# Kernel optimization log

Measured on AMD Instinct MI355X. Metric: run time of the kernel, lower is better.

## Reference

```python
import jax, jax.numpy as jnp
import numpy as np

HEADS = 8
DIM_HEAD = 64
EPS = 1e-5  # fp32 eps in ChanLayerNorm


def chan_layer_norm(x, g):
    # x: [b, c, h, w]; normalize over channel dim with biased variance
    mean = jnp.mean(x, axis=1, keepdims=True)
    var = jnp.var(x, axis=1, keepdims=True)
    return (x - mean) * jax.lax.rsqrt(var + EPS) * g[None, :, None, None]


def setup_inputs() -> dict:
    key = jax.random.key(0)
    k1, k2, k3 = jax.random.split(key, 3)
    dim, inner = 512, HEADS * DIM_HEAD
    fmap = jax.random.normal(k1, (16, dim, 64, 64), dtype=jnp.float32)
    # 1x1 conv weights (no bias); scaled like typical init to keep softmax unsaturated
    w_qkv = jax.random.normal(k2, (3 * inner, dim), dtype=jnp.float32) * 0.02
    w_out = jax.random.normal(k3, (dim, inner), dtype=jnp.float32) * 0.02
    g1 = jnp.ones((dim,), dtype=jnp.float32)
    g2 = jnp.ones((dim,), dtype=jnp.float32)
    return {"fmap": fmap, "g1": g1, "w_qkv": w_qkv, "w_out": w_out, "g2": g2}


def reference(fmap, g1, w_qkv, w_out, g2):
    b, c, X, Y = fmap.shape
    h, dh = HEADS, DIM_HEAD
    n = X * Y  # seq_len
    scale = dh ** -0.5

    x = chan_layer_norm(fmap, g1)
    # 1x1 conv == channel matmul: [b, 3*inner, X, Y]
    qkv = jnp.einsum('bcxy,oc->boxy', x, w_qkv)
    q, k, v = jnp.split(qkv, 3, axis=1)

    def to_bhnc(t):
        # b (h c) x y -> b h n c
        return t.reshape(b, h, dh, n).transpose(0, 1, 3, 2)

    q, k, v = map(to_bhnc, (q, k, v))

    q = jax.nn.softmax(q, axis=-1) * scale          # softmax over feature dim
    k = jax.nn.softmax(k, axis=2)                   # softmax over seq dim
    v = v / jnp.linalg.norm(v, axis=-1, keepdims=True)  # l2norm
    inv_sqrt_n = 1.0 / np.sqrt(n)
    k = k * inv_sqrt_n
    v = v * inv_sqrt_n

    context = jnp.einsum('bhnd,bhne->bhde', k, v)   # small d x e context
    out = jnp.einsum('bhnd,bhde->bhne', q, context)  # [b, h, n, dh]

    # b h n d -> b (h d) x y
    out = out.transpose(0, 1, 3, 2).reshape(b, h * dh, X, Y)
    out = jax.nn.gelu(out, approximate=False)
    out = jnp.einsum('bcxy,oc->boxy', out, w_out)
    return chan_layer_norm(out, g2)
```

## Files before the change

### kernel.cpp

```cpp
#include <hip/hip_runtime.h>

typedef unsigned short u16;
typedef __attribute__((ext_vector_type(2))) float f32x2;
typedef __attribute__((ext_vector_type(4))) float f32x4;
typedef __attribute__((ext_vector_type(8))) short s16x8;
typedef __attribute__((ext_vector_type(8))) u16 u16x8;
typedef __attribute__((ext_vector_type(4))) u16 u16x4;

#define NB 16
#define CD 512
#define NS 4096
#define NHD 8

#define SBAR  __builtin_amdgcn_s_barrier()
#define SCHED __builtin_amdgcn_sched_barrier(0)
#define LGKM0 asm volatile("s_waitcnt lgkmcnt(0)" ::: "memory")
#define PRIO1 __builtin_amdgcn_s_setprio(1)
#define PRIO0 __builtin_amdgcn_s_setprio(0)

__device__ __forceinline__ float bf2f(u16 u){
  union { unsigned int i; float f; } z; z.i = ((unsigned int)u) << 16; return z.f;
}
__device__ __forceinline__ u16 f2bf(float f){
  union { float f; unsigned int i; } z; z.f = f;
  unsigned int i = z.i;
  return (u16)((i + 0x7fffu + ((i >> 16) & 1u)) >> 16);
}
__device__ __forceinline__ float gelu_f(float x){
  return 0.5f * x * (1.0f + erff(x * 0.70710678118654752440f));
}
__device__ __forceinline__ void gl_lds16(const u16* g, u16* l){
  __builtin_amdgcn_global_load_lds((const __attribute__((address_space(1))) void*)(g),
                                   (__attribute__((address_space(3))) void*)(l), 16, 0, 0);
}

__global__ void prep_w_k(const float* __restrict__ wqkv, const float* __restrict__ g1,
                         const float* __restrict__ wout, u16* __restrict__ w1b,
                         u16* __restrict__ w2b){
  int i = blockIdx.x * 256 + threadIdx.x;
  if (i < 1536*512) {
    w1b[i] = f2bf(wqkv[i] * g1[i & 511]);
  } else {
    int j = i - 1536*512;
    w2b[j] = f2bf(wout[j]);
  }
}

__global__ __launch_bounds__(512) void ln1t_k(const float* __restrict__ fmap,
                                              u16* __restrict__ xlnT){
  int b = blockIdx.y, n0 = blockIdx.x * 32;
  int t = threadIdx.x;
  int lane = t & 63, wv = t >> 6;
  __shared__ float Lb[512][36];
  __shared__ u16 Tt[64][36];
  __shared__ float red1[8][8][4], red2[8][8][4];
  __shared__ float mean_s[32], rstd_s[32];

  int ng = t & 7;
  float s1[4] = {0,0,0,0}, s2[4] = {0,0,0,0};
  const float* fb = fmap + ((size_t)b*CD)*NS + n0 + ng*4;
  #pragma unroll
  for (int it = 0; it < 8; ++it){
    int q = it*512 + t;
    int c = q >> 3;
    f32x4 v = *(const f32x4*)&fb[(size_t)c*NS];
    *(f32x4*)&Lb[c][ng*4] = v;
    #pragma unroll
    for (int j = 0; j < 4; ++j){ s1[j] += v[j]; s2[j] += v[j]*v[j]; }
  }
  #pragma unroll
  for (int off = 8; off < 64; off <<= 1)
    #pragma unroll
    for (int j = 0; j < 4; ++j){
      s1[j] += __shfl_xor(s1[j], off, 64);
      s2[j] += __shfl_xor(s2[j], off, 64);
    }
  if (lane < 8){
    #pragma unroll
    for (int j = 0; j < 4; ++j){ red1[wv][lane][j] = s1[j]; red2[wv][lane][j] = s2[j]; }
  }
  __syncthreads();
  if (t < 32){
    int g = t >> 2, j = t & 3;
    float a = 0.f, bq = 0.f;
    #pragma unroll
    for (int w = 0; w < 8; ++w){ a += red1[w][g][j]; bq += red2[w][g][j]; }
    float mn = a * (1.f/512.f);
    float var = bq * (1.f/512.f) - mn*mn;
    mean_s[t] = mn; rstd_s[t] = rsqrtf(var + 1e-5f);
  }
  __syncthreads();

  for (int ct = 0; ct < 8; ++ct){
    {
      int cl = t >> 3, n4 = (t & 7) * 4;
      f32x4 v = *(const f32x4*)&Lb[ct*64 + cl][n4];
      u16x4 pk;
      #pragma unroll
      for (int j = 0; j < 4; ++j)
        pk[j] = f2bf((v[j] - mean_s[n4+j]) * rstd_s[n4+j]);
      *(u16x4*)&Tt[cl][n4] = pk;
    }
    __syncthreads();
    {
      int nr = t >> 4, c4 = t & 15;
      u16x4 w;
      #pragma unroll
      for (int j = 0; j < 4; ++j) w[j] = Tt[c4*4 + j][nr];
      *(u16x4*)&xlnT[((size_t)b*NS + n0 + nr)*CD + ct*64 + c4*4] = w;
    }
    __syncthreads();
  }
}

__global__ __launch_bounds__(512, 2) void gemm1_k(const u16* __restrict__ A,
                                                  const u16* __restrict__ Bm,
                                                  u16* __restrict__ Cm){
  __shared__ u16 lds[4][16384];
  int bi = blockIdx.x;
  int xcd = bi & 7, r2 = bi >> 3;
  int gi = r2 / 6, yy = r2 - gi*6;
  int g  = gi*8 + xcd;
  int x  = g & 15, z = g >> 4;
  int o0 = yy*256, bn0 = x*256;
  int t = threadIdx.x;
  int lane = t & 63, wv = t >> 6;
  int wm = wv >> 2, wn = wv & 3;
  int fr = lane & 15, fg = lane >> 4;
  const u16* Ab = A + (size_t)o0*512;
  const u16* Bb = Bm + ((size_t)z*NS + bn0)*512;
  int rA = t >> 2, cx = t & 3;

  f32x4 acc[8][4];
  #pragma unroll
  for (int i=0;i<8;++i)
    #pragma unroll
    for (int j=0;j<4;++j) acc[i][j] = (f32x4){0.f,0.f,0.f,0.f};
  s16x8 afr[4], bfr[4];

  auto stA = [&](int slot, int kt, int bt){
    int r = bt*128 + rA;
    gl_lds16(Ab + (size_t)r*512 + kt + ((cx ^ (r&3))<<3), &lds[slot][bt*4096 + wv*512]);
  };
  auto stB = [&](int slot, int kt, int bt){
    int r = bt*128 + rA;
    gl_lds16(Bb + (size_t)r*512 + kt + ((cx ^ (r&3))<<3), &lds[slot][8192 + bt*4096 + wv*512]);
  };
  auto ldA = [&](int slot, int h){
    #pragma unroll
    for (int mi=0;mi<4;++mi){
      int R = wm*128 + (h*4+mi)*16 + fr;
      afr[mi] = *(const s16x8*)&lds[slot][R*32 + ((fg ^ (R&3))<<3)];
    }
  };
  auto ldB = [&](int slot){
    #pragma unroll
    for (int nj=0;nj<4;++nj){
      int R = wn*64 + nj*16 + fr;
      bfr[nj] = *(const s16x8*)&lds[slot][8192 + R*32 + ((fg ^ (R&3))<<3)];
    }
  };
  auto mm16 = [&](int h){
    #pragma unroll
    for (int mi=0;mi<4;++mi)
      #pragma unroll
      for (int nj=0;nj<4;++nj)
        acc[h*4+mi][nj] = __builtin_amdgcn_mfma_f32_16x16x32_bf16(
            afr[mi], bfr[nj], acc[h*4+mi][nj], 0,0,0);
  };

  #pragma unroll
  for (int p=0;p<3;++p){ stA(p,p*32,0); stB(p,p*32,0); stA(p,p*32,1); stB(p,p*32,1); }
  asm volatile("s_waitcnt vmcnt(8)" ::: "memory");
  SBAR; SCHED;

  #pragma unroll
  for (int kt=0; kt<16; ++kt){
    int slot = kt & 3, ns = (kt+3) & 3, kn = (kt+3)*32;
    ldA(slot,0); ldB(slot);
    if (kt<13){ stA(ns,kn,0); stB(ns,kn,0); }
    SBAR; LGKM0; SCHED;
    PRIO1; mm16(0); PRIO0;
    SBAR; SCHED;
    ldA(slot,1);
    if (kt<13){ stA(ns,kn,1); stB(ns,kn,1); }
    SBAR; LGKM0; SCHED;
    PRIO1; mm16(1); PRIO0;
    if (kt<13)       asm volatile("s_waitcnt vmcnt(8)" ::: "memory");
    else if (kt==13) asm volatile("s_waitcnt vmcnt(4)" ::: "memory");
    else if (kt==14) asm volatile("s_waitcnt vmcnt(0)" ::: "memory");
    SBAR; SCHED;
  }

  size_t cb = (size_t)z * 1536 * NS;
  #pragma unroll
  for (int mi=0;mi<8;++mi)
    #pragma unroll
    for (int nj=0;nj<4;++nj){
      int row = o0 + wm*128 + mi*16 + fg*4;
      int col = bn0 + wn*64 + nj*16 + fr;
      #pragma unroll
      for (int r=0;r<4;++r)
        Cm[cb + (size_t)(row+r)*NS + col] = f2bf(acc[mi][nj][r]);
    }
}

__global__ __launch_bounds__(512, 2) void gemm2ln_k(const u16* __restrict__ A,
                                                    const u16* __restrict__ Bm,
                                                    const float* __restrict__ g2,
                                                    float* __restrict__ out){
  __shared__ u16 lds[3][20480];
  int x = blockIdx.x, z = blockIdx.y;
  int n0 = x*128;
  int t = threadIdx.x;
  int lane = t & 63, wv = t >> 6;
  int wm = wv >> 1, wn = wv & 1;
  int fr = lane & 15, fg = lane >> 4;
  const u16* Ab = A;
  const u16* Bb = Bm + ((size_t)z*NS + n0)*512;
  int rA = t >> 2, cx = t & 3;

  f32x4 acc[8][4];
  #pragma unroll
  for (int i=0;i<8;++i)
    #pragma unroll
    for (int j=0;j<4;++j) acc[i][j] = (f32x4){0.f,0.f,0.f,0.f};
  s16x8 afr[4], bfr[4];

  auto stA = [&](int slot, int kt, int bt){
    int r = bt*128 + rA;
    gl_lds16(Ab + (size_t)r*512 + kt + ((cx ^ (r&3))<<3), &lds[slot][bt*4096 + wv*512]);
  };
  auto stB = [&](int slot, int kt){
    int r = rA;
    gl_lds16(Bb + (size_t)r*512 + kt + ((cx ^ (r&3))<<3), &lds[slot][16384 + wv*512]);
  };
  auto ldA = [&](int slot, int h){
    #pragma unroll
    for (int mi=0;mi<4;++mi){
      int R = wm*128 + (h*4+mi)*16 + fr;
      afr[mi] = *(const s16x8*)&lds[slot][R*32 + ((fg ^ (R&3))<<3)];
    }
  };
  auto ldB = [&](int slot){
    #pragma unroll
    for (int nj=0;nj<4;++nj){
      int R = wn*64 + nj*16 + fr;
      bfr[nj] = *(const s16x8*)&lds[slot][16384 + R*32 + ((fg ^ (R&3))<<3)];
    }
  };
  auto mm16 = [&](int h){
    #pragma unroll
    for (int mi=0;mi<4;++mi)
      #pragma unroll
      for (int nj=0;nj<4;++nj)
        acc[h*4+mi][nj] = __builtin_amdgcn_mfma_f32_16x16x32_bf16(
            afr[mi], bfr[nj], acc[h*4+mi][nj], 0,0,0);
  };

  #pragma unroll
  for (int p=0;p<2;++p){ stA(p,p*32,0); stA(p,p*32,1); stB(p,p*32); stA(p,p*32,2); stA(p,p*32,3); }
  asm volatile("s_waitcnt vmcnt(5)" ::: "memory");
  SBAR; SCHED;

  #pragma unroll
  for (int kt=0; kt<16; ++kt){
    int slot = kt%3, ns = (kt+2)%3, kn = (kt+2)*32;
    ldA(slot,0); ldB(slot);
    if (kt<14){ stA(ns,kn,0); stA(ns,kn,1); stB(ns,kn); }
    SBAR; LGKM0; SCHED;
    PRIO1; mm16(0); PRIO0;
    SBAR; SCHED;
    ldA(slot,1);
    if (kt<14){ stA(ns,kn,2); stA(ns,kn,3); }
    SBAR; LGKM0; SCHED;
    PRIO1; mm16(1); PRIO0;
    if (kt<14)       asm volatile("s_waitcnt vmcnt(5)" ::: "memory");
    else if (kt==14) asm volatile("s_waitcnt vmcnt(0)" ::: "memory");
    SBAR; SCHED;
  }

  __syncthreads();
  float* red1 = (float*)&lds[0][0];
  float* red2 = red1 + 512;
  float* ms   = red2 + 512;
  float* rs   = ms + 128;
  float s1[4], s2[4];
  #pragma unroll
  for (int nj=0;nj<4;++nj){
    float a = 0.f, b2 = 0.f;
    #pragma unroll
    for (int mi=0;mi<8;++mi)
      #pragma unroll
      for (int r=0;r<4;++r){ float v = acc[mi][nj][r]; a += v; b2 += v*v; }
    s1[nj] = a; s2[nj] = b2;
  }
  #pragma unroll
  for (int off=16; off<64; off<<=1)
    #pragma unroll
    for (int nj=0;nj<4;++nj){
      s1[nj] += __shfl_xor(s1[nj], off, 64);
      s2[nj] += __shfl_xor(s2[nj], off, 64);
    }
  if (fg == 0){
    #pragma unroll
    for (int nj=0;nj<4;++nj){
      int c = wn*64 + nj*16 + fr;
      red1[wm*128 + c] = s1[nj];
      red2[wm*128 + c] = s2[nj];
    }
  }
  __syncthreads();
  if (t < 128){
    float a  = red1[t] + red1[128+t] + red1[256+t] + red1[384+t];
    float b2 = red2[t] + red2[128+t] + red2[256+t] + red2[384+t];
    float mn = a * (1.f/512.f);
    float var = b2 * (1.f/512.f) - mn*mn;
    ms[t] = mn; rs[t] = rsqrtf(var + 1e-5f);
  }
  __syncthreads();
  float mc[4], rc[4];
  #pragma unroll
  for (int nj=0;nj<4;++nj){
    int c = wn*64 + nj*16 + fr;
    mc[nj] = ms[c]; rc[nj] = rs[c];
  }
  float* ob = out + (size_t)z*CD*NS + n0;
  #pragma unroll
  for (int mi=0;mi<8;++mi)
    #pragma unroll
    for (int r=0;r<4;++r){
      int row = wm*128 + mi*16 + fg*4 + r;
      float gg = g2[row];
      #pragma unroll
      for (int nj=0;nj<4;++nj)
        ob[(size_t)row*NS + wn*64 + nj*16 + fr] = (acc[mi][nj][r] - mc[nj])*rc[nj]*gg;
    }
}

__global__ __launch_bounds__(256) void ctxpart_k(const u16* __restrict__ qkv,
                                                 float* __restrict__ part,
                                                 float* __restrict__ mS){
  int chunk = blockIdx.x, bh = blockIdx.y;
  int b = bh >> 3, h = bh & 7;
  int t = threadIdx.x;
  int lane = t & 63, wv = t >> 6;
  int fr = lane & 15, fg = lane >> 4;
  __shared__ u16 KT[64*128];
  __shared__ u16 VT[64*128];
  __shared__ float invn_s[128];
  const u16* kb = qkv + ((size_t)(b*1536 + 512  + h*64))*NS;
  const u16* vb = qkv + ((size_t)(b*1536 + 1024 + h*64))*NS;
  int d = t >> 2, q = t & 3;

  float mloc = -3.0e38f;
  #pragma unroll
  for (int nt = 0; nt < 4; ++nt)
    #pragma unroll
    for (int s = 0; s < 4; ++s){
      u16x8 kk = *(const u16x8*)&kb[(size_t)d*NS + chunk*512 + nt*128 + q*32 + s*8];
      #pragma unroll
      for (int j = 0; j < 8; ++j) mloc = fmaxf(mloc, bf2f(kk[j]));
    }
  mloc = fmaxf(mloc, __shfl_xor(mloc, 1, 64));
  mloc = fmaxf(mloc, __shfl_xor(mloc, 2, 64));
  float sloc = 0.f;

  f32x4 acc[4][4];
  #pragma unroll
  for (int i=0;i<4;++i)
    #pragma unroll
    for (int j=0;j<4;++j) acc[i][j] = (f32x4){0.f,0.f,0.f,0.f};

  for (int nt = 0; nt < 4; ++nt){
    int n0 = chunk*512 + nt*128;
    if (nt) __syncthreads();
    u16x8 kreg[4];
    #pragma unroll
    for (int s = 0; s < 4; ++s){
      int c0 = q*32 + s*8;
      u16x8 vv = *(const u16x8*)&vb[(size_t)d*NS + n0 + c0];
      *(u16x8*)&VT[d*128 + (c0 ^ ((d&7)<<3))] = vv;
      kreg[s] = *(const u16x8*)&kb[(size_t)d*NS + n0 + c0];
    }
    __syncthreads();
    if (t < 128){
      float ss = 0.f;
      #pragma unroll
      for (int e = 0; e < 64; ++e){
        float xv = bf2f(VT[e*128 + (t ^ ((e&7)<<3))]);
        ss += xv*xv;
      }
      invn_s[t] = rsqrtf(ss);
    }
    __syncthreads();
    #pragma unroll
    for (int s = 0; s < 4; ++s){
      int c0 = q*32 + s*8;
      u16x8 kk = kreg[s];
      u16x8 ek;
      #pragma unroll
      for (int j = 0; j < 8; ++j){
        float e = __expf(bf2f(kk[j]) - mloc);
        sloc += e;
        ek[j] = f2bf(e * invn_s[c0 + j]);
      }
      *(u16x8*)&KT[d*128 + (c0 ^ ((d&7)<<3))] = ek;
    }
    __syncthreads();
    int kc = wv*32 + fg*8;
    s16x8 af[4], bfr[4];
    #pragma unroll
    for (int i=0;i<4;++i){
      int ra = i*16 + fr;
      af[i]  = *(const s16x8*)&KT[ra*128 + (kc ^ ((ra&7)<<3))];
      bfr[i] = *(const s16x8*)&VT[ra*128 + (kc ^ ((ra&7)<<3))];
    }
    #pragma unroll
    for (int i=0;i<4;++i)
      #pragma unroll
      for (int j=0;j<4;++j)
        acc[i][j] = __builtin_amdgcn_mfma_f32_16x16x32_bf16(af[i], bfr[j], acc[i][j], 0,0,0);
  }

  sloc += __shfl_xor(sloc, 1, 64);
  sloc += __shfl_xor(sloc, 2, 64);
  if (q == 0){
    size_t mb = ((size_t)bh*8 + chunk)*128;
    mS[mb + d]      = mloc;
    mS[mb + 64 + d] = sloc;
  }

  float* buf0 = (float*)KT;
  float* buf1 = (float*)VT;
  auto dump = [&](float* bf){
    #pragma unroll
    for (int i=0;i<4;++i)
      #pragma unroll
      for (int j=0;j<4;++j)
        #pragma unroll
        for (int r=0;r<4;++r) bf[((i*4+j)*4+r)*64 + lane] = acc[i][j][r];
  };
  auto addin = [&](float* bf){
    #pragma unroll
    for (int i=0;i<4;++i)
      #pragma unroll
      for (int j=0;j<4;++j)
        #pragma unroll
        for (int r=0;r<4;++r) acc[i][j][r] += bf[((i*4+j)*4+r)*64 + lane];
  };
  __syncthreads();
  if (wv==1) dump(buf0);
  if (wv==3) dump(buf1);
  __syncthreads();
  if (wv==0) addin(buf0);
  if (wv==2) addin(buf1);
  __syncthreads();
  if (wv==2) dump(buf0);
  __syncthreads();
  if (wv==0){
    addin(buf0);
    float* pp = part + ((size_t)bh*8 + chunk)*4096;
    #pragma unroll
    for (int i=0;i<4;++i)
      #pragma unroll
      for (int j=0;j<4;++j)
        #pragma unroll
        for (int r=0;r<4;++r)
          pp[(i*16+fg*4+r)*64 + j*16+fr] = acc[i][j][r];
  }
}

__global__ void ctxred_k(const float* __restrict__ part, const float* __restrict__ mS,
                         float* __restrict__ ctx){
  int bh = blockIdx.x, t = threadIdx.x;
  __shared__ float fs[8][64];
  if (t < 64){
    int d = t;
    float mc[8];
    float mx = -3.0e38f;
    #pragma unroll
    for (int c=0;c<8;++c){ mc[c] = mS[((size_t)bh*8 + c)*128 + d]; mx = fmaxf(mx, mc[c]); }
    float es[8]; float denom = 0.f;
    #pragma unroll
    for (int c=0;c<8;++c){
      es[c] = __expf(mc[c] - mx);
      denom += es[c] * mS[((size_t)bh*8 + c)*128 + 64 + d];
    }
    float inv = 1.0f / (denom * 4096.0f);
    #pragma unroll
    for (int c=0;c<8;++c) fs[c][d] = es[c] * inv;
  }
  __syncthreads();
  #pragma unroll
  for (int i=0;i<16;++i){
    int idx = t + i*256;
    int d = idx >> 6;
    float s = 0.f;
    #pragma unroll
    for (int ch=0; ch<8; ++ch) s += fs[ch][d] * part[((size_t)bh*8 + ch)*4096 + idx];
    ctx[(size_t)bh*4096 + idx] = s;
  }
}

__global__ __launch_bounds__(256) void attnout_k(const u16* __restrict__ qkv,
                                                 const float* __restrict__ ctx,
                                                 u16* __restrict__ gT){
  int bh = blockIdx.y;
  int b = bh >> 3, h = bh & 7;
  int n0 = blockIdx.x * 256;
  int t = threadIdx.x;
  int lane = t & 63, wv = t >> 6;
  int fr = lane & 15, fg = lane >> 4;
  __shared__ u16 P[256][72];
  __shared__ u16 cT[64][72];

  const float* cs = ctx + (size_t)bh*4096;
  #pragma unroll
  for (int i=0;i<16;++i){
    int idx = i*256 + t;
    int d = idx >> 6, e = idx & 63;
    cT[e][d] = f2bf(cs[idx]);
  }

  const u16* qb = qkv + ((size_t)(b*1536 + h*64))*NS + n0 + t;
  float p[64];
  #pragma unroll
  for (int d=0; d<64; ++d) p[d] = bf2f(qb[(size_t)d*NS]);
  float m = p[0];
  #pragma unroll
  for (int d=1; d<64; ++d) m = fmaxf(m, p[d]);
  float s = 0.f;
  #pragma unroll
  for (int d=0; d<64; ++d){ p[d] = __expf(p[d]-m); s += p[d]; }
  float inv = 0.125f / s;
  #pragma unroll
  for (int d0=0; d0<8; ++d0){
    u16x8 pk;
    #pragma unroll
    for (int j=0;j<8;++j) pk[j] = f2bf(p[d0*8+j] * inv);
    *(u16x8*)&P[t][d0*8] = pk;
  }
  __syncthreads();

  f32x4 acc[4][4];
  #pragma unroll
  for (int i=0;i<4;++i)
    #pragma unroll
    for (int j=0;j<4;++j) acc[i][j] = (f32x4){0.f,0.f,0.f,0.f};
  #pragma unroll
  for (int k=0; k<2; ++k){
    s16x8 af[4], bfr[4];
    #pragma unroll
    for (int i=0;i<4;++i){
      af[i]  = *(const s16x8*)&P[wv*64 + i*16 + fr][k*32 + fg*8];
      bfr[i] = *(const s16x8*)&cT[i*16 + fr][k*32 + fg*8];
    }
    #pragma unroll
    for (int i=0;i<4;++i)
      #pragma unroll
      for (int j=0;j<4;++j)
        acc[i][j] = __builtin_amdgcn_mfma_f32_16x16x32_bf16(af[i], bfr[j], acc[i][j], 0,0,0);
  }

  #pragma unroll
  for (int i=0;i<4;++i)
    #pragma unroll
    for (int j=0;j<4;++j)
      #pragma unroll
      for (int r=0;r<4;++r)
        P[wv*64 + i*16 + fg*4 + r][j*16 + fr] = f2bf(gelu_f(acc[i][j][r]));

  int sub = lane >> 4, e4 = (lane & 15) * 4;
  #pragma unroll
  for (int it=0; it<16; ++it){
    int row = wv*64 + it*4 + sub;
    *(u16x4*)&gT[((size_t)b*NS + n0 + row)*CD + h*64 + e4] = *(u16x4*)&P[row][e4];
  }
}

extern "C" void kernel_launch(void* const* d_in, const int* in_sizes, int n_in,
                              void* d_out, int out_size, void* d_ws, size_t ws_size,
                              hipStream_t stream) {
  const float* fmap = (const float*)d_in[0];
  const float* g1   = (const float*)d_in[1];
  const float* wqkv = (const float*)d_in[2];
  const float* wout = (const float*)d_in[3];
  const float* g2   = (const float*)d_in[4];
  float* out = (float*)d_out;

  char* ws = (char*)d_ws;
  size_t off = 0;
  auto alloc = [&](size_t bytes) -> void* {
    void* p = ws + off;
    off += (bytes + 255) & ~(size_t)255;
    return p;
  };
  u16*   qkv  = (u16*)alloc((size_t)16*1536*4096*2);
  u16*   xlnT = (u16*)alloc((size_t)16*4096*512*2);
  u16*   gT   = xlnT;
  float* part = (float*)alloc((size_t)128*8*4096*4);
  float* mS   = (float*)alloc((size_t)128*8*128*4);
  float* ctx  = (float*)alloc((size_t)128*4096*4);
  u16*   w1b  = (u16*)alloc((size_t)1536*512*2);
  u16*   w2b  = (u16*)alloc((size_t)512*512*2);
  if (off > ws_size) return;

  prep_w_k<<<4096, 256, 0, stream>>>(wqkv, g1, wout, w1b, w2b);
  ln1t_k<<<dim3(128,16), 512, 0, stream>>>(fmap, xlnT);
  gemm1_k<<<1536, 512, 0, stream>>>(w1b, xlnT, qkv);
  ctxpart_k<<<dim3(8,128), 256, 0, stream>>>(qkv, part, mS);
  ctxred_k<<<128, 256, 0, stream>>>(part, mS, ctx);
  attnout_k<<<dim3(16,128), 256, 0, stream>>>(qkv, ctx, gT);
  gemm2ln_k<<<dim3(32,16), 512, 0, stream>>>(w2b, gT, g2, out);
}
```

Measured before the change: 343.1 us.

## Shrink gemm1 tiles to 128x256 for higher occupancy and change LDS swizzles

The QKV projection GEMM is retiled from 256x256 to 128x256 output tiles, which doubles the grid to 3072 blocks. It cuts the LDS ring from four stages to three and halves the accumulators so that four blocks can be resident per CU. The block-to-XCD mapping now groups batches per XCD, and a new 8-chunk XOR swizzle is used for the 64-wide K tile layout. gemm2ln also gets a stronger 4-way swizzle to reduce LDS bank conflicts. The trade-off is lower operand reuse per tile and a shallower prefetch pipeline, in exchange for more latency hiding through occupancy.

```diff
diff --git a/kernel.cpp b/kernel.cpp
--- a/kernel.cpp
+++ b/kernel.cpp
@@ -113,91 +113,96 @@
   }
 }
 
-__global__ __launch_bounds__(512, 2) void gemm1_k(const u16* __restrict__ A,
+__global__ __launch_bounds__(512, 4) void gemm1_k(const u16* __restrict__ A,
                                                   const u16* __restrict__ Bm,
                                                   u16* __restrict__ Cm){
-  __shared__ u16 lds[4][16384];
+  __shared__ u16 lds[3][12288];
   int bi = blockIdx.x;
   int xcd = bi & 7, r2 = bi >> 3;
-  int gi = r2 / 6, yy = r2 - gi*6;
-  int g  = gi*8 + xcd;
-  int x  = g & 15, z = g >> 4;
-  int o0 = yy*256, bn0 = x*256;
+  int oo  = r2 % 12;
+  int x   = (r2 / 12) & 15;
+  int zl  = r2 / 192;
+  int z   = xcd*2 + zl;
+  int o0 = oo*128, bn0 = x*256;
   int t = threadIdx.x;
   int lane = t & 63, wv = t >> 6;
   int wm = wv >> 2, wn = wv & 3;
   int fr = lane & 15, fg = lane >> 4;
   const u16* Ab = A + (size_t)o0*512;
   const u16* Bb = Bm + ((size_t)z*NS + bn0)*512;
-  int rA = t >> 2, cx = t & 3;
-
-  f32x4 acc[8][4];
-  #pragma unroll
-  for (int i=0;i<8;++i)
+
+  int l8  = lane >> 3;
+  int c8l = (lane & 7) ^ l8;
+  int shf = c8l >> 2;
+  int sc  = (c8l & 3) * 8;
+
+  f32x4 acc[4][4];
+  #pragma unroll
+  for (int i=0;i<4;++i)
     #pragma unroll
     for (int j=0;j<4;++j) acc[i][j] = (f32x4){0.f,0.f,0.f,0.f};
   s16x8 afr[4], bfr[4];
 
-  auto stA = [&](int slot, int kt, int bt){
-    int r = bt*128 + rA;
-    gl_lds16(Ab + (size_t)r*512 + kt + ((cx ^ (r&3))<<3), &lds[slot][bt*4096 + wv*512]);
-  };
-  auto stB = [&](int slot, int kt, int bt){
-    int r = bt*128 + rA;
-    gl_lds16(Bb + (size_t)r*512 + kt + ((cx ^ (r&3))<<3), &lds[slot][8192 + bt*4096 + wv*512]);
-  };
-  auto ldA = [&](int slot, int h){
+  auto stA = [&](int slot, int kt){
+    int L = wv*8 + l8;
+    int r = shf*64 + L;
+    gl_lds16(Ab + (size_t)r*512 + kt + sc, &lds[slot][wv*512]);
+  };
+  auto stB = [&](int slot, int kt, int i){
+    int L = i*64 + wv*8 + l8;
+    int r = shf*128 + L;
+    gl_lds16(Bb + (size_t)r*512 + kt + sc, &lds[slot][4096 + i*4096 + wv*512]);
+  };
+  auto ldA = [&](int slot){
     #pragma unroll
     for (int mi=0;mi<4;++mi){
-      int R = wm*128 + (h*4+mi)*16 + fr;
-      afr[mi] = *(const s16x8*)&lds[slot][R*32 + ((fg ^ (R&3))<<3)];
+      int L  = mi*16 + fr;
+      int c8 = (wm*4 + fg) ^ (L & 7);
+      afr[mi] = *(const s16x8*)&lds[slot][L*64 + c8*8];
     }
   };
   auto ldB = [&](int slot){
     #pragma unroll
     for (int nj=0;nj<4;++nj){
-      int R = wn*64 + nj*16 + fr;
-      bfr[nj] = *(const s16x8*)&lds[slot][8192 + R*32 + ((fg ^ (R&3))<<3)];
-    }
-  };
-  auto mm16 = [&](int h){
+      int L  = (wn&1)*64 + nj*16 + fr;
+      int c8 = ((wn>>1)*4 + fg) ^ (L & 7);
+      bfr[nj] = *(const s16x8*)&lds[slot][4096 + L*64 + c8*8];
+    }
+  };
+
+  stA(0,0);  stB(0,0,0);  stB(0,0,1);
+  stA(1,32); stB(1,32,0); stB(1,32,1);
+  asm volatile("s_waitcnt vmcnt(3)" ::: "memory");
+  SBAR; SCHED;
+
+  #pragma unroll
+  for (int kt=0; kt<16; ++kt){
+    int slot = kt % 3;
+    ldA(slot); ldB(slot);
+    if (kt < 14){
+      int ns = (kt+2)%3, kn = (kt+2)*32;
+      stA(ns,kn); stB(ns,kn,0); stB(ns,kn,1);
+    }
+    LGKM0; SCHED;
+    PRIO1;
     #pragma unroll
     for (int mi=0;mi<4;++mi)
       #pragma unroll
       for (int nj=0;nj<4;++nj)
-        acc[h*4+mi][nj] = __builtin_amdgcn_mfma_f32_16x16x32_bf16(
-            afr[mi], bfr[nj], acc[h*4+mi][nj], 0,0,0);
-  };
-
-  #pragma unroll
-  for (int p=0;p<3;++p){ stA(p,p*32,0); stB(p,p*32,0); stA(p,p*32,1); stB(p,p*32,1); }
-  asm volatile("s_waitcnt vmcnt(8)" ::: "memory");
-  SBAR; SCHED;
-
-  #pragma unroll
-  for (int kt=0; kt<16; ++kt){
-    int slot = kt & 3, ns = (kt+3) & 3, kn = (kt+3)*32;
-    ldA(slot,0); ldB(slot);
-    if (kt<13){ stA(ns,kn,0); stB(ns,kn,0); }
-    SBAR; LGKM0; SCHED;
-    PRIO1; mm16(0); PRIO0;
+        acc[mi][nj] = __builtin_amdgcn_mfma_f32_16x16x32_bf16(
+            afr[mi], bfr[nj], acc[mi][nj], 0,0,0);
+    PRIO0;
+    if (kt < 14)       asm volatile("s_waitcnt vmcnt(3)" ::: "memory");
+    else if (kt == 14) asm volatile("s_waitcnt vmcnt(0)" ::: "memory");
     SBAR; SCHED;
-    ldA(slot,1);
-    if (kt<13){ stA(ns,kn,1); stB(ns,kn,1); }
-    SBAR; LGKM0; SCHED;
-    PRIO1; mm16(1); PRIO0;
-    if (kt<13)       asm volatile("s_waitcnt vmcnt(8)" ::: "memory");
-    else if (kt==13) asm volatile("s_waitcnt vmcnt(4)" ::: "memory");
-    else if (kt==14) asm volatile("s_waitcnt vmcnt(0)" ::: "memory");
-    SBAR; SCHED;
   }
 
   size_t cb = (size_t)z * 1536 * NS;
   #pragma unroll
-  for (int mi=0;mi<8;++mi)
+  for (int mi=0;mi<4;++mi)
     #pragma unroll
     for (int nj=0;nj<4;++nj){
-      int row = o0 + wm*128 + mi*16 + fg*4;
+      int row = o0 + wm*64 + mi*16 + fg*4;
       int col = bn0 + wn*64 + nj*16 + fr;
       #pragma unroll
       for (int r=0;r<4;++r)
@@ -227,26 +232,27 @@
     for (int j=0;j<4;++j) acc[i][j] = (f32x4){0.f,0.f,0.f,0.f};
   s16x8 afr[4], bfr[4];
 
+  auto swz4 = [](int c, int r){ return (c ^ (r & 3) ^ ((r >> 2) & 3)) & 3; };
   auto stA = [&](int slot, int kt, int bt){
     int r = bt*128 + rA;
-    gl_lds16(Ab + (size_t)r*512 + kt + ((cx ^ (r&3))<<3), &lds[slot][bt*4096 + wv*512]);
+    gl_lds16(Ab + (size_t)r*512 + kt + (swz4(cx,r)<<3), &lds[slot][bt*4096 + wv*512]);
   };
   auto stB = [&](int slot, int kt){
     int r = rA;
-    gl_lds16(Bb + (size_t)r*512 + kt + ((cx ^ (r&3))<<3), &lds[slot][16384 + wv*512]);
+    gl_lds16(Bb + (size_t)r*512 + kt + (swz4(cx,r)<<3), &lds[slot][16384 + wv*512]);
   };
   auto ldA = [&](int slot, int h){
     #pragma unroll
     for (int mi=0;mi<4;++mi){
       int R = wm*128 + (h*4+mi)*16 + fr;
-      afr[mi] = *(const s16x8*)&lds[slot][R*32 + ((fg ^ (R&3))<<3)];
+      afr[mi] = *(const s16x8*)&lds[slot][R*32 + (swz4(fg,R)<<3)];
     }
   };
   auto ldB = [&](int slot){
     #pragma unroll
     for (int nj=0;nj<4;++nj){
       int R = wn*64 + nj*16 + fr;
-      bfr[nj] = *(const s16x8*)&lds[slot][16384 + R*32 + ((fg ^ (R&3))<<3)];
+      bfr[nj] = *(const s16x8*)&lds[slot][16384 + R*32 + (swz4(fg,R)<<3)];
     }
   };
   auto mm16 = [&](int h){
@@ -608,7 +614,7 @@
 
   prep_w_k<<<4096, 256, 0, stream>>>(wqkv, g1, wout, w1b, w2b);
   ln1t_k<<<dim3(128,16), 512, 0, stream>>>(fmap, xlnT);
-  gemm1_k<<<1536, 512, 0, stream>>>(w1b, xlnT, qkv);
+  gemm1_k<<<3072, 512, 0, stream>>>(w1b, xlnT, qkv);
   ctxpart_k<<<dim3(8,128), 256, 0, stream>>>(qkv, part, mS);
   ctxred_k<<<128, 256, 0, stream>>>(part, mS, ctx);
   attnout_k<<<dim3(16,128), 256, 0, stream>>>(qkv, ctx, gT);
```

Result: faster. 336.2 us (-2.0%).
